# Kernel tuning notes

Measured on AMD Instinct MI355X. Metric: run time of the kernel, lower is better.

## Reference

```python
import jax, jax.numpy as jnp
import numpy as np

B, S, FEA, T = 32, 8, 2560, 800   # batch, speakers, feature dim (20*128), time frames
N_CLUSTERS, EMB = 512, 256        # speaker-embedding dictionary shape (m)
H = 8                             # n_heads


def setup_inputs() -> dict:
    key = jax.random.key(0)
    ks = jax.random.split(key, 9)
    x = jax.random.normal(ks[0], (B, FEA, T), dtype=jnp.float32)
    mask = jax.random.uniform(ks[1], (B, S, T), dtype=jnp.float32)
    # learned params
    W_w = jax.random.normal(ks[2], (H, FEA), dtype=jnp.float32) * 0.02
    W_b = jnp.zeros((H,), dtype=jnp.float32)
    U_w = jax.random.normal(ks[3], (H, EMB), dtype=jnp.float32) * 0.02
    U_b = jnp.zeros((H,), dtype=jnp.float32)
    v_w = jax.random.normal(ks[4], (1, H), dtype=jnp.float32) * 0.1
    v_b = jnp.zeros((1,), dtype=jnp.float32)
    # speaker-embedding dictionary (self.m loaded from .npy)
    m = jax.random.normal(ks[5], (N_CLUSTERS, EMB), dtype=jnp.float32)
    return {"x": x, "mask": mask, "W_w": W_w, "W_b": W_b,
            "U_w": U_w, "U_b": U_b, "v_w": v_w, "v_b": v_b, "m": m}


def reference(x, mask, W_w, W_b, U_w, U_b, v_w, v_b, m):
    # masked mean-pool over time: (B,S,Fea) -- avoids the torch .repeat blowup
    pooled = jnp.einsum('bft,bst->bsf', x, mask)
    denom = jnp.sum(mask, axis=2)[..., None] + 1e-10   # (B,S,1)
    x2 = pooled / denom                                 # (B,S,Fea)
    # additive attention scores over clusters
    w = x2 @ W_w.T + W_b                                # (B,S,H)
    u = m @ U_w.T + U_b                                 # (N,H)
    s = jnp.tanh(w[:, :, None, :] + u[None, None, :, :])  # (B,S,N,H)
    c = jnp.einsum('bsnh,h->bsn', s, v_w[0]) + v_b[0]   # (B,S,N)
    a = jax.nn.sigmoid(c)
    # gated weighted sum of cluster embeddings
    e = jnp.einsum('bsn,ne->bse', a, m)                 # (B,S,Emb)
    return e
```

## Files before the change

### kernel.cpp

```cpp
#include <hip/hip_runtime.h>
#include <hip/hip_bf16.h>
#include <math.h>

#define B 32
#define S 8
#define FEA 2560
#define T 800
#define NCL 512
#define EMB 256
#define H 8

#define BF 64
#define SEC 128
#define NSEC 6
#define XTILE 16384
#define MROWB 1664

typedef __attribute__((ext_vector_type(8))) short bf16x8;
typedef __attribute__((ext_vector_type(4))) float f32x4;

__device__ __forceinline__ short4 cvt_bf16x4(float4 v) {
    union { short4 s4; __hip_bfloat162 h[2]; } u;
    u.h[0] = __float22bfloat162_rn(make_float2(v.x, v.y));
    u.h[1] = __float22bfloat162_rn(make_float2(v.z, v.w));
    return u.s4;
}

__global__ __launch_bounds__(256) void pool_u_kernel(const float* __restrict__ x,
                                                     const float* __restrict__ mask,
                                                     const float* __restrict__ U_w,
                                                     const float* __restrict__ U_b,
                                                     const float* __restrict__ m,
                                                     float* __restrict__ pooled,
                                                     float* __restrict__ u_out) {
    const int b = blockIdx.y;

    if (blockIdx.x == FEA / BF) {
        if (b >= 8) return;
        const int n  = b * 64 + (threadIdx.x >> 2);
        const int h0 = (threadIdx.x & 3) * 2;
        float a0 = 0.f, a1 = 0.f;
        #pragma unroll 4
        for (int e = 0; e < EMB; ++e) {
            const float mv = m[n * EMB + e];
            a0 += mv * U_w[h0 * EMB + e];
            a1 += mv * U_w[(h0 + 1) * EMB + e];
        }
        u_out[n * H + h0]     = a0 + U_b[h0];
        u_out[n * H + h0 + 1] = a1 + U_b[h0 + 1];
        return;
    }

    __shared__ short mask_l[S * (MROWB / 2)];
    __shared__ short xls[XTILE];

    const int tid = threadIdx.x;
    const int f0  = blockIdx.x * BF;
    const float* xb = x + (size_t)b * FEA * T;

    float4 R[8];

    #pragma unroll
    for (int r = 0; r < 8; ++r) {
        const int row = r * 8 + (tid >> 5), c4 = tid & 31;
        R[r] = *(const float4*)(xb + (size_t)(f0 + row) * T + c4 * 4);
    }

    for (int v = tid; v < S * 200; v += 256) {
        const int s = v / 200, c4 = v % 200;
        const float4 mv = *(const float4*)(mask + ((size_t)(b * S + s)) * T + c4 * 4);
        const int byte = s * MROWB + ((c4 * 8) ^ (s << 4));
        *(short4*)((char*)mask_l + byte) = cvt_bf16x4(mv);
    }

    #pragma unroll
    for (int r = 0; r < 8; ++r) {
        const int row = r * 8 + (tid >> 5), c4 = tid & 31;
        *(short4*)((char*)xls + row * 256 + ((c4 * 8) ^ ((row & 7) << 4))) = cvt_bf16x4(R[r]);
    }
    #pragma unroll
    for (int r = 0; r < 8; ++r) {
        const int row = r * 8 + (tid >> 5), c4 = tid & 31;
        R[r] = *(const float4*)(xb + (size_t)(f0 + row) * T + SEC + c4 * 4);
    }
    __syncthreads();

    const int wave = tid >> 6, lane = tid & 63;
    const int kb16 = (lane >> 4) * 16;
    const int xrow = wave * 16 + (lane & 15);
    const int xswz = (xrow & 7) << 4;
    const int srow = (lane & 15) & 7;
    const int mbase = srow * MROWB;
    const int mswz = srow << 4;

    f32x4 acc = {0.f, 0.f, 0.f, 0.f};

    #pragma unroll
    for (int sec = 0; sec < NSEC; ++sec) {
        const int bufb = (sec & 1) * XTILE;
        #pragma unroll
        for (int st = 0; st < 4; ++st) {
            const int xb_ = bufb + xrow * 256 + ((st * 64 + kb16) ^ xswz);
            const bf16x8 bx = *(const bf16x8*)((const char*)xls + xb_);
            const int mb_ = mbase + (((sec * 4 + st) * 64 + kb16) ^ mswz);
            const bf16x8 am = *(const bf16x8*)((const char*)mask_l + mb_);
            acc = __builtin_amdgcn_mfma_f32_16x16x32_bf16(am, bx, acc, 0, 0, 0);
        }
        if (sec < NSEC - 1) {
            const int wb = ((sec + 1) & 1) * XTILE;
            #pragma unroll
            for (int r = 0; r < 8; ++r) {
                const int row = r * 8 + (tid >> 5), c4 = tid & 31;
                *(short4*)((char*)xls + wb + row * 256 + ((c4 * 8) ^ ((row & 7) << 4)))
                    = cvt_bf16x4(R[r]);
            }
            if (sec < NSEC - 2) {
                #pragma unroll
                for (int r = 0; r < 8; ++r) {
                    const int row = r * 8 + (tid >> 5), c4 = tid & 31;
                    R[r] = *(const float4*)(xb + (size_t)(f0 + row) * T + (sec + 2) * SEC + c4 * 4);
                }
            }
        }
        __syncthreads();
    }

    {
        const float* xt = xb + (size_t)(f0 + xrow) * T + 768 + (lane >> 4) * 8;
        const float4 t0 = *(const float4*)(xt);
        const float4 t1 = *(const float4*)(xt + 4);
        union { bf16x8 v; short4 s4[2]; } Bx;
        Bx.s4[0] = cvt_bf16x4(t0);
        Bx.s4[1] = cvt_bf16x4(t1);
        const int mb_ = mbase + ((24 * 64 + kb16) ^ mswz);
        const bf16x8 am = *(const bf16x8*)((const char*)mask_l + mb_);
        acc = __builtin_amdgcn_mfma_f32_16x16x32_bf16(am, Bx.v, acc, 0, 0, 0);
    }

    if (lane < 32) {
        const int col = lane & 15;
        #pragma unroll
        for (int i = 0; i < 4; ++i) {
            const int sr = (lane >> 4) * 4 + i;
            pooled[(size_t)(b * S + sr) * FEA + f0 + wave * 16 + col] = acc[i];
        }
    }
}

__global__ __launch_bounds__(256) void wden_kernel(const float* __restrict__ pooled,
                                                   const float* __restrict__ mask,
                                                   const float* __restrict__ W_w,
                                                   const float* __restrict__ W_b,
                                                   float* __restrict__ w_out) {
    __shared__ float red[256];
    __shared__ float wred[4][8];
    const int bs  = blockIdx.x;
    const int tid = threadIdx.x;

    float p = 0.f;
    for (int t = tid; t < T; t += 256) p += mask[(size_t)bs * T + t];
    red[tid] = p;
    __syncthreads();
    for (int st = 128; st > 0; st >>= 1) {
        if (tid < st) red[tid] += red[tid + st];
        __syncthreads();
    }
    const float inv_d = 1.f / (red[0] + 1e-10f);

    float acc[8];
    #pragma unroll
    for (int h = 0; h < 8; ++h) acc[h] = 0.f;
    for (int f = tid; f < FEA; f += 256) {
        const float xv = pooled[(size_t)bs * FEA + f] * inv_d;
        #pragma unroll
        for (int h = 0; h < 8; ++h) acc[h] += xv * W_w[h * FEA + f];
    }
    const int lane = tid & 63, wave = tid >> 6;
    #pragma unroll
    for (int h = 0; h < 8; ++h) {
        float v = acc[h];
        #pragma unroll
        for (int off = 32; off > 0; off >>= 1) v += __shfl_xor(v, off, 64);
        if (lane == 0) wred[wave][h] = v;
    }
    __syncthreads();
    if (tid < 8)
        w_out[bs * H + tid] = wred[0][tid] + wred[1][tid] + wred[2][tid] + wred[3][tid] + W_b[tid];
}

__global__ __launch_bounds__(256) void gate_kernel(const float* __restrict__ w_buf,
                                                   const float* __restrict__ u_buf,
                                                   const float* __restrict__ v_w,
                                                   const float* __restrict__ v_b,
                                                   float* __restrict__ a_out,
                                                   float* __restrict__ out) {
    const int idx = blockIdx.x * 256 + threadIdx.x;
    if (idx < B * S * EMB) out[idx] = 0.f;
    const int bs = idx >> 9, n = idx & 511;
    float c = v_b[0];
    #pragma unroll
    for (int h = 0; h < 8; ++h)
        c += tanhf(w_buf[bs * H + h] + u_buf[n * H + h]) * v_w[h];
    a_out[idx] = 1.f / (1.f + expf(-c));
}

__global__ __launch_bounds__(256) void egemv_kernel(const float* __restrict__ a_buf,
                                                    const float* __restrict__ m,
                                                    float* __restrict__ out) {
    __shared__ float a_sh[256];
    const int bs = blockIdx.x >> 1, half = blockIdx.x & 1;
    const int tid = threadIdx.x;
    a_sh[tid] = a_buf[bs * NCL + half * 256 + tid];
    __syncthreads();
    float acc = 0.f;
    #pragma unroll 8
    for (int n = 0; n < 256; ++n)
        acc += a_sh[n] * m[(half * 256 + n) * EMB + tid];
    atomicAdd(&out[bs * EMB + tid], acc);
}

extern "C" void kernel_launch(void* const* d_in, const int* in_sizes, int n_in,
                              void* d_out, int out_size, void* d_ws, size_t ws_size,
                              hipStream_t stream) {
    const float* x    = (const float*)d_in[0];
    const float* mask = (const float*)d_in[1];
    const float* W_w  = (const float*)d_in[2];
    const float* W_b  = (const float*)d_in[3];
    const float* U_w  = (const float*)d_in[4];
    const float* U_b  = (const float*)d_in[5];
    const float* v_w  = (const float*)d_in[6];
    const float* v_b  = (const float*)d_in[7];
    const float* m    = (const float*)d_in[8];
    float* out = (float*)d_out;

    float* ws     = (float*)d_ws;
    float* pooled = ws;
    float* u_buf  = pooled + B * S * FEA;
    float* w_buf  = u_buf + NCL * H;
    float* a_buf  = w_buf + B * S * H;

    pool_u_kernel<<<dim3(FEA / BF + 1, B), 256, 0, stream>>>(
        x, mask, U_w, U_b, m, pooled, u_buf);
    wden_kernel<<<B * S, 256, 0, stream>>>(pooled, mask, W_w, W_b, w_buf);
    gate_kernel<<<B * S * NCL / 256, 256, 0, stream>>>(w_buf, u_buf, v_w, v_b, a_buf, out);
    egemv_kernel<<<B * S * 2, 256, 0, stream>>>(a_buf, m, out);
}
```

Before: 75.24 us.

## Give each wave private double-buffered x tiles and drop block-wide barriers

Each of the four waves now loads, converts and stages only its own 16 feature rows into a private pair of LDS buffers, instead of sharing one block-wide tile. This removes the per-section __syncthreads from the pooling loop. Two register sets are kept so global loads run two sections ahead of the MFMA work, putting more memory traffic in flight. The cost is more live VGPRs for the doubled prefetch registers, which may lower occupancy, and it relies on LDS reads and writes within one wave completing in program order.

New measurement: 75.13 us. Within noise of the previous version (-0.1%).

```diff
diff --git a/kernel.cpp b/kernel.cpp
--- a/kernel.cpp
+++ b/kernel.cpp
@@ -13,7 +13,7 @@
 #define BF 64
 #define SEC 128
 #define NSEC 6
-#define XTILE 16384
+#define WVB 4096
 #define MROWB 1664
 
 typedef __attribute__((ext_vector_type(8))) short bf16x8;
@@ -24,6 +24,36 @@
     u.h[0] = __float22bfloat162_rn(make_float2(v.x, v.y));
     u.h[1] = __float22bfloat162_rn(make_float2(v.z, v.w));
     return u.s4;
+}
+
+__device__ __forceinline__ void load_sec_w(const float* __restrict__ xw, int sec,
+                                           int lane, float4 R[8]) {
+    const int c4 = lane & 31;
+    #pragma unroll
+    for (int r = 0; r < 8; ++r) {
+        const int row = r * 2 + (lane >> 5);
+        R[r] = *(const float4*)(xw + (size_t)row * T + sec * SEC + c4 * 4);
+    }
+}
+
+__device__ __forceinline__ void write_sec_w(char* __restrict__ buf, int lane, const float4 R[8]) {
+    const int c4 = lane & 31;
+    #pragma unroll
+    for (int r = 0; r < 8; ++r) {
+        const int row = r * 2 + (lane >> 5);
+        *(short4*)(buf + row * 256 + ((c4 * 8) ^ ((row & 7) << 4))) = cvt_bf16x4(R[r]);
+    }
+}
+
+#define STEP4(secv, bufp) {                                                          \
+    _Pragma("unroll")                                                                \
+    for (int st_ = 0; st_ < 4; ++st_) {                                              \
+        const bf16x8 bx_ = *(const bf16x8*)((bufp) + xrow * 256                      \
+                              + ((st_ * 64 + kb16) ^ xswz));                         \
+        const bf16x8 am_ = *(const bf16x8*)((const char*)mask_l + mbase              \
+                              + ((((secv) * 4 + st_) * 64 + kb16) ^ mswz));          \
+        acc = __builtin_amdgcn_mfma_f32_16x16x32_bf16(am_, bx_, acc, 0, 0, 0);       \
+    }                                                                                \
 }
 
 __global__ __launch_bounds__(256) void pool_u_kernel(const float* __restrict__ x,
@@ -52,19 +82,20 @@
     }
 
     __shared__ short mask_l[S * (MROWB / 2)];
-    __shared__ short xls[XTILE];
-
-    const int tid = threadIdx.x;
-    const int f0  = blockIdx.x * BF;
-    const float* xb = x + (size_t)b * FEA * T;
-
-    float4 R[8];
-
-    #pragma unroll
-    for (int r = 0; r < 8; ++r) {
-        const int row = r * 8 + (tid >> 5), c4 = tid & 31;
-        R[r] = *(const float4*)(xb + (size_t)(f0 + row) * T + c4 * 4);
-    }
+    __shared__ char  xls[4 * 2 * WVB];
+
+    const int tid  = threadIdx.x;
+    const int wave = tid >> 6, lane = tid & 63;
+    const int f0   = blockIdx.x * BF;
+
+    const float* xw = x + ((size_t)b * FEA + f0 + wave * 16) * T;
+    char* buf0 = xls + wave * 2 * WVB;
+    char* buf1 = buf0 + WVB;
+
+    float4 R0[8], R1[8];
+
+    load_sec_w(xw, 0, lane, R0);
+    load_sec_w(xw, 1, lane, R1);
 
     for (int v = tid; v < S * 200; v += 256) {
         const int s = v / 200, c4 = v % 200;
@@ -72,68 +103,43 @@
         const int byte = s * MROWB + ((c4 * 8) ^ (s << 4));
         *(short4*)((char*)mask_l + byte) = cvt_bf16x4(mv);
     }
-
-    #pragma unroll
-    for (int r = 0; r < 8; ++r) {
-        const int row = r * 8 + (tid >> 5), c4 = tid & 31;
-        *(short4*)((char*)xls + row * 256 + ((c4 * 8) ^ ((row & 7) << 4))) = cvt_bf16x4(R[r]);
-    }
-    #pragma unroll
-    for (int r = 0; r < 8; ++r) {
-        const int row = r * 8 + (tid >> 5), c4 = tid & 31;
-        R[r] = *(const float4*)(xb + (size_t)(f0 + row) * T + SEC + c4 * 4);
-    }
-    __syncthreads();
-
-    const int wave = tid >> 6, lane = tid & 63;
+    __syncthreads();
+
+    write_sec_w(buf0, lane, R0);
+    load_sec_w(xw, 2, lane, R0);
+    write_sec_w(buf1, lane, R1);
+    load_sec_w(xw, 3, lane, R1);
+
     const int kb16 = (lane >> 4) * 16;
-    const int xrow = wave * 16 + (lane & 15);
+    const int xrow = lane & 15;
     const int xswz = (xrow & 7) << 4;
-    const int srow = (lane & 15) & 7;
+    const int srow = lane & 7;
     const int mbase = srow * MROWB;
     const int mswz = srow << 4;
 
     f32x4 acc = {0.f, 0.f, 0.f, 0.f};
 
-    #pragma unroll
-    for (int sec = 0; sec < NSEC; ++sec) {
-        const int bufb = (sec & 1) * XTILE;
-        #pragma unroll
-        for (int st = 0; st < 4; ++st) {
-            const int xb_ = bufb + xrow * 256 + ((st * 64 + kb16) ^ xswz);
-            const bf16x8 bx = *(const bf16x8*)((const char*)xls + xb_);
-            const int mb_ = mbase + (((sec * 4 + st) * 64 + kb16) ^ mswz);
-            const bf16x8 am = *(const bf16x8*)((const char*)mask_l + mb_);
-            acc = __builtin_amdgcn_mfma_f32_16x16x32_bf16(am, bx, acc, 0, 0, 0);
-        }
-        if (sec < NSEC - 1) {
-            const int wb = ((sec + 1) & 1) * XTILE;
-            #pragma unroll
-            for (int r = 0; r < 8; ++r) {
-                const int row = r * 8 + (tid >> 5), c4 = tid & 31;
-                *(short4*)((char*)xls + wb + row * 256 + ((c4 * 8) ^ ((row & 7) << 4)))
-                    = cvt_bf16x4(R[r]);
-            }
-            if (sec < NSEC - 2) {
-                #pragma unroll
-                for (int r = 0; r < 8; ++r) {
-                    const int row = r * 8 + (tid >> 5), c4 = tid & 31;
-                    R[r] = *(const float4*)(xb + (size_t)(f0 + row) * T + (sec + 2) * SEC + c4 * 4);
-                }
-            }
-        }
-        __syncthreads();
-    }
+    #pragma unroll 1
+    for (int st = 0; st < 4; st += 2) {
+        STEP4(st, buf0)
+        write_sec_w(buf0, lane, R0);
+        if (st + 4 < NSEC) load_sec_w(xw, st + 4, lane, R0);
+        STEP4(st + 1, buf1)
+        write_sec_w(buf1, lane, R1);
+        if (st + 5 < NSEC) load_sec_w(xw, st + 5, lane, R1);
+    }
+    STEP4(4, buf0)
+    STEP4(5, buf1)
 
     {
-        const float* xt = xb + (size_t)(f0 + xrow) * T + 768 + (lane >> 4) * 8;
+        const float* xt = xw + (size_t)xrow * T + 768 + (lane >> 4) * 8;
         const float4 t0 = *(const float4*)(xt);
         const float4 t1 = *(const float4*)(xt + 4);
         union { bf16x8 v; short4 s4[2]; } Bx;
         Bx.s4[0] = cvt_bf16x4(t0);
         Bx.s4[1] = cvt_bf16x4(t1);
-        const int mb_ = mbase + ((24 * 64 + kb16) ^ mswz);
-        const bf16x8 am = *(const bf16x8*)((const char*)mask_l + mb_);
+        const bf16x8 am = *(const bf16x8*)((const char*)mask_l + mbase
+                              + ((24 * 64 + kb16) ^ mswz));
         acc = __builtin_amdgcn_mfma_f32_16x16x32_bf16(am, Bx.v, acc, 0, 0, 0);
     }
 
```

## Widen x staging to 256-column pairs and fuse gate into egemv kernel

Applied to the files above, without the earlier changes.

The pooling kernel now stages x in two 128-column halves (256 columns per stage), so the main loop runs three pair stages with fewer barriers instead of six 128-column sections. Each thread now holds 16 float4 prefetch registers, which raises register pressure. The gate computation (tanh/sigmoid) moves into the egemv kernel, and zeroing of the output moves into wden. This removes one kernel launch and the a_buf round trip through global memory.

Result: no change. 75.99 us (+1.0%).

```diff
diff --git a/kernel.cpp b/kernel.cpp
--- a/kernel.cpp
+++ b/kernel.cpp
@@ -11,9 +11,8 @@
 #define H 8
 
 #define BF 64
-#define SEC 128
-#define NSEC 6
-#define XTILE 16384
+#define PAIRB 256
+#define XHALF 16384
 #define MROWB 1664
 
 typedef __attribute__((ext_vector_type(8))) short bf16x8;
@@ -25,6 +24,33 @@
     u.h[1] = __float22bfloat162_rn(make_float2(v.z, v.w));
     return u.s4;
 }
+
+#define LOAD_PAIR(p) {                                                              \
+    _Pragma("unroll")                                                               \
+    for (int r = 0; r < 16; ++r)                                                    \
+        R[r] = *(const float4*)(xb + (size_t)(f0 + r * 4 + lrow) * T                \
+                                + (p) * PAIRB + lc4);                               \
+}
+
+#define WRITE_PAIR() {                                                              \
+    _Pragma("unroll")                                                               \
+    for (int r = 0; r < 16; ++r) {                                                  \
+        const int row_ = r * 4 + lrow;                                              \
+        *(short4*)(xls + whalf * XHALF + row_ * 256 + (wb8 ^ ((row_ & 7) << 4)))    \
+            = cvt_bf16x4(R[r]);                                                     \
+    }                                                                               \
+}
+
+#define CSTEP(p, st) {                                                              \
+    const bf16x8 bx_ = *(const bf16x8*)(xls + ((st) >> 2) * XHALF + xrow * 256      \
+                          + ((((st) & 3) * 64 + kb16) ^ xswz));                     \
+    const bf16x8 am_ = *(const bf16x8*)((const char*)mask_l + mbase                 \
+                          + ((((p) * 8 + (st)) * 64 + kb16) ^ mswz));               \
+    acc = __builtin_amdgcn_mfma_f32_16x16x32_bf16(am_, bx_, acc, 0, 0, 0);          \
+}
+
+#define CPAIR(p) { CSTEP(p,0) CSTEP(p,1) CSTEP(p,2) CSTEP(p,3)                      \
+                   CSTEP(p,4) CSTEP(p,5) CSTEP(p,6) CSTEP(p,7) }
 
 __global__ __launch_bounds__(256) void pool_u_kernel(const float* __restrict__ x,
                                                      const float* __restrict__ mask,
@@ -52,19 +78,20 @@
     }
 
     __shared__ short mask_l[S * (MROWB / 2)];
-    __shared__ short xls[XTILE];
+    __shared__ char  xls[2 * XHALF];
 
     const int tid = threadIdx.x;
     const int f0  = blockIdx.x * BF;
     const float* xb = x + (size_t)b * FEA * T;
 
-    float4 R[8];
-
-    #pragma unroll
-    for (int r = 0; r < 8; ++r) {
-        const int row = r * 8 + (tid >> 5), c4 = tid & 31;
-        R[r] = *(const float4*)(xb + (size_t)(f0 + row) * T + c4 * 4);
-    }
+    const int lrow = tid >> 6;
+    const int lc4  = (tid & 63) * 4;
+    const int whalf = (tid & 63) >> 5;
+    const int wb8   = (tid & 31) * 8;
+
+    float4 R[16];
+
+    LOAD_PAIR(0)
 
     for (int v = tid; v < S * 200; v += 256) {
         const int s = v / 200, c4 = v % 200;
@@ -73,57 +100,32 @@
         *(short4*)((char*)mask_l + byte) = cvt_bf16x4(mv);
     }
 
-    #pragma unroll
-    for (int r = 0; r < 8; ++r) {
-        const int row = r * 8 + (tid >> 5), c4 = tid & 31;
-        *(short4*)((char*)xls + row * 256 + ((c4 * 8) ^ ((row & 7) << 4))) = cvt_bf16x4(R[r]);
-    }
-    #pragma unroll
-    for (int r = 0; r < 8; ++r) {
-        const int row = r * 8 + (tid >> 5), c4 = tid & 31;
-        R[r] = *(const float4*)(xb + (size_t)(f0 + row) * T + SEC + c4 * 4);
-    }
+    WRITE_PAIR()
+    LOAD_PAIR(1)
     __syncthreads();
 
     const int wave = tid >> 6, lane = tid & 63;
     const int kb16 = (lane >> 4) * 16;
     const int xrow = wave * 16 + (lane & 15);
     const int xswz = (xrow & 7) << 4;
-    const int srow = (lane & 15) & 7;
+    const int srow = lane & 7;
     const int mbase = srow * MROWB;
     const int mswz = srow << 4;
 
     f32x4 acc = {0.f, 0.f, 0.f, 0.f};
 
-    #pragma unroll
-    for (int sec = 0; sec < NSEC; ++sec) {
-        const int bufb = (sec & 1) * XTILE;
-        #pragma unroll
-        for (int st = 0; st < 4; ++st) {
-            const int xb_ = bufb + xrow * 256 + ((st * 64 + kb16) ^ xswz);
-            const bf16x8 bx = *(const bf16x8*)((const char*)xls + xb_);
-            const int mb_ = mbase + (((sec * 4 + st) * 64 + kb16) ^ mswz);
-            const bf16x8 am = *(const bf16x8*)((const char*)mask_l + mb_);
-            acc = __builtin_amdgcn_mfma_f32_16x16x32_bf16(am, bx, acc, 0, 0, 0);
-        }
-        if (sec < NSEC - 1) {
-            const int wb = ((sec + 1) & 1) * XTILE;
-            #pragma unroll
-            for (int r = 0; r < 8; ++r) {
-                const int row = r * 8 + (tid >> 5), c4 = tid & 31;
-                *(short4*)((char*)xls + wb + row * 256 + ((c4 * 8) ^ ((row & 7) << 4)))
-                    = cvt_bf16x4(R[r]);
-            }
-            if (sec < NSEC - 2) {
-                #pragma unroll
-                for (int r = 0; r < 8; ++r) {
-                    const int row = r * 8 + (tid >> 5), c4 = tid & 31;
-                    R[r] = *(const float4*)(xb + (size_t)(f0 + row) * T + (sec + 2) * SEC + c4 * 4);
-                }
-            }
-        }
-        __syncthreads();
-    }
+    CPAIR(0)
+    __syncthreads();
+    WRITE_PAIR()
+    LOAD_PAIR(2)
+    __syncthreads();
+
+    CPAIR(1)
+    __syncthreads();
+    WRITE_PAIR()
+    __syncthreads();
+
+    CPAIR(2)
 
     {
         const float* xt = xb + (size_t)(f0 + xrow) * T + 768 + (lane >> 4) * 8;
@@ -132,8 +134,8 @@
         union { bf16x8 v; short4 s4[2]; } Bx;
         Bx.s4[0] = cvt_bf16x4(t0);
         Bx.s4[1] = cvt_bf16x4(t1);
-        const int mb_ = mbase + ((24 * 64 + kb16) ^ mswz);
-        const bf16x8 am = *(const bf16x8*)((const char*)mask_l + mb_);
+        const bf16x8 am = *(const bf16x8*)((const char*)mask_l + mbase
+                              + ((24 * 64 + kb16) ^ mswz));
         acc = __builtin_amdgcn_mfma_f32_16x16x32_bf16(am, Bx.v, acc, 0, 0, 0);
     }
 
@@ -151,11 +153,14 @@
                                                    const float* __restrict__ mask,
                                                    const float* __restrict__ W_w,
                                                    const float* __restrict__ W_b,
-                                                   float* __restrict__ w_out) {
+                                                   float* __restrict__ w_out,
+                                                   float* __restrict__ out) {
     __shared__ float red[256];
     __shared__ float wred[4][8];
     const int bs  = blockIdx.x;
     const int tid = threadIdx.x;
+
+    out[bs * EMB + tid] = 0.f;
 
     float p = 0.f;
     for (int t = tid; t < T; t += 256) p += mask[(size_t)bs * T + t];
@@ -188,34 +193,28 @@
         w_out[bs * H + tid] = wred[0][tid] + wred[1][tid] + wred[2][tid] + wred[3][tid] + W_b[tid];
 }
 
-__global__ __launch_bounds__(256) void gate_kernel(const float* __restrict__ w_buf,
-                                                   const float* __restrict__ u_buf,
-                                                   const float* __restrict__ v_w,
-                                                   const float* __restrict__ v_b,
-                                                   float* __restrict__ a_out,
-                                                   float* __restrict__ out) {
-    const int idx = blockIdx.x * 256 + threadIdx.x;
-    if (idx < B * S * EMB) out[idx] = 0.f;
-    const int bs = idx >> 9, n = idx & 511;
-    float c = v_b[0];
-    #pragma unroll
-    for (int h = 0; h < 8; ++h)
-        c += tanhf(w_buf[bs * H + h] + u_buf[n * H + h]) * v_w[h];
-    a_out[idx] = 1.f / (1.f + expf(-c));
-}
-
-__global__ __launch_bounds__(256) void egemv_kernel(const float* __restrict__ a_buf,
+__global__ __launch_bounds__(256) void egemv_kernel(const float* __restrict__ w_buf,
+                                                    const float* __restrict__ u_buf,
+                                                    const float* __restrict__ v_w,
+                                                    const float* __restrict__ v_b,
                                                     const float* __restrict__ m,
                                                     float* __restrict__ out) {
     __shared__ float a_sh[256];
     const int bs = blockIdx.x >> 1, half = blockIdx.x & 1;
     const int tid = threadIdx.x;
-    a_sh[tid] = a_buf[bs * NCL + half * 256 + tid];
-    __syncthreads();
+    const int n = half * 256 + tid;
+
+    float c = v_b[0];
+    #pragma unroll
+    for (int h = 0; h < 8; ++h)
+        c += tanhf(w_buf[bs * H + h] + u_buf[n * H + h]) * v_w[h];
+    a_sh[tid] = 1.f / (1.f + expf(-c));
+    __syncthreads();
+
     float acc = 0.f;
     #pragma unroll 8
-    for (int n = 0; n < 256; ++n)
-        acc += a_sh[n] * m[(half * 256 + n) * EMB + tid];
+    for (int n2 = 0; n2 < 256; ++n2)
+        acc += a_sh[n2] * m[(half * 256 + n2) * EMB + tid];
     atomicAdd(&out[bs * EMB + tid], acc);
 }
 
@@ -237,11 +236,9 @@
     float* pooled = ws;
     float* u_buf  = pooled + B * S * FEA;
     float* w_buf  = u_buf + NCL * H;
-    float* a_buf  = w_buf + B * S * H;
 
     pool_u_kernel<<<dim3(FEA / BF + 1, B), 256, 0, stream>>>(
         x, mask, U_w, U_b, m, pooled, u_buf);
-    wden_kernel<<<B * S, 256, 0, stream>>>(pooled, mask, W_w, W_b, w_buf);
-    gate_kernel<<<B * S * NCL / 256, 256, 0, stream>>>(w_buf, u_buf, v_w, v_b, a_buf, out);
-    egemv_kernel<<<B * S * 2, 256, 0, stream>>>(a_buf, m, out);
-}
+    wden_kernel<<<B * S, 256, 0, stream>>>(pooled, mask, W_w, W_b, w_buf, out);
+    egemv_kernel<<<B * S * 2, 256, 0, stream>>>(w_buf, u_buf, v_w, v_b, m, out);
+}
```
